# Optimization experiments

Hardware: AMD Instinct MI355X
Metric: run time of the kernel (lower is better)

Reference implementation:

```python
import jax, jax.numpy as jnp
import numpy as np

B, S, C, H = 2, 4096, 1024, 16
DH = C // H  # 64
# diffusers: attn.scale = dim_head ** -0.5; code divides scores by scale**0.5
SCALE = 1.0 / (float(DH) ** -0.25)  # == DH ** 0.25


def setup_inputs() -> dict:
    key = jax.random.key(0)
    ks = jax.random.split(key, 6)
    w = 0.02
    return {
        "hidden_states": jax.random.normal(ks[0], (B, S, C), jnp.float32),
        "Wq": jax.random.normal(ks[1], (C, C), jnp.float32) * w,
        "Wk": jax.random.normal(ks[2], (C, C), jnp.float32) * w,
        "Wv": jax.random.normal(ks[3], (C, C), jnp.float32) * w,
        "Wo": jax.random.normal(ks[4], (C, C), jnp.float32) * w,
        "bo": jnp.zeros((C,), jnp.float32),
        # token sizes >= 1 (number of patches each token represents)
        "token_sizes": jax.random.randint(ks[5], (B, S), 1, 17, jnp.int32),
    }


def _split_heads(x):
    # [B, S, C] -> [B, H, S, DH]
    return x.reshape(B, S, H, DH).transpose(0, 2, 1, 3)


def reference(hidden_states, Wq, Wk, Wv, Wo, bo, token_sizes):
    q = _split_heads(hidden_states @ Wq)  # [B,H,S,DH]
    k = _split_heads(hidden_states @ Wk)
    v = _split_heads(hidden_states @ Wv)
    # QK^T with diffusers-style scaling: scores / attn.scale**0.5 == scores * DH**0.25
    scores = jnp.einsum("bhqd,bhkd->bhqk", q, k) * SCALE  # [B,H,S,S]
    # additive log(token_size) bias over keys (self-attention path)
    log_sizes = jnp.log(token_sizes.astype(jnp.float32))  # [B,S]
    scores = scores + log_sizes[:, None, None, :]
    probs = jax.nn.softmax(scores, axis=-1)
    out = jnp.einsum("bhqk,bhkd->bhqd", probs, v)  # [B,H,S,DH]
    out = out.transpose(0, 2, 1, 3).reshape(B, S, C)  # merge heads
    return out @ Wo + bo  # to_out[0] linear; to_out[1] dropout is identity
```

## Files before the change

### kernel.cpp

```cpp
#include <hip/hip_runtime.h>


typedef unsigned short u16;
typedef unsigned int u32;
typedef _Float16 f16x8 __attribute__((ext_vector_type(8)));
typedef float f32x4 __attribute__((ext_vector_type(4)));
typedef short short4v __attribute__((ext_vector_type(4)));

constexpr int SEQ = 4096, CDIM = 1024, NH = 16, DHE = 64;
constexpr float SCALE2 = 2.8284271247461903f * 1.4426950408889634f;

template <int N> struct IC { static constexpr int v = N; };

union Frag { f16x8 v; short4v h[2]; };

__device__ __forceinline__ u16 f2h(float f) {
  union { _Float16 h; u16 u; } x;
  x.h = (_Float16)f;
  return x.u;
}

__device__ __forceinline__ u32 pkrtz(float a, float b) {
  u32 r;
  asm("v_cvt_pkrtz_f16_f32 %0, %1, %2" : "=v"(r) : "v"(a), "v"(b));
  return r;
}

__device__ __forceinline__ short4v pk4(const f32x4& v) {
  union { u32 w[2]; short4v s; } u;
  u.w[0] = pkrtz(v[0], v[1]);
  u.w[1] = pkrtz(v[2], v[3]);
  return u.s;
}

__device__ __forceinline__ float exp2fast(float x) {
  float r;
  asm("v_exp_f32 %0, %1" : "=v"(r) : "v"(x));
  return r;
}

__device__ __forceinline__ f32x4 mfma16(const Frag& a, const Frag& b, f32x4 c) {
  return __builtin_amdgcn_mfma_f32_16x16x32_f16(a.v, b.v, c, 0, 0, 0);
}

__device__ __forceinline__ void gl16(const void* g, void* l) {
  __builtin_amdgcn_global_load_lds(
      (const __attribute__((address_space(1))) u32*)g,
      (__attribute__((address_space(3))) u32*)l, 16, 0, 0);
}


__global__ void cast_x_kernel(const float* __restrict__ x, u16* __restrict__ out) {
  size_t i = ((size_t)blockIdx.x * 256 + threadIdx.x) * 8;
  float4 a = *(const float4*)(x + i);
  float4 b = *(const float4*)(x + i + 4);
  uint4 o;
  o.x = (u32)f2h(a.x) | ((u32)f2h(a.y) << 16);
  o.y = (u32)f2h(a.z) | ((u32)f2h(a.w) << 16);
  o.z = (u32)f2h(b.x) | ((u32)f2h(b.y) << 16);
  o.w = (u32)f2h(b.z) | ((u32)f2h(b.w) << 16);
  *(uint4*)(out + i) = o;
}

__global__ __launch_bounds__(256) void transpose_w4_kernel(
    const float* __restrict__ Wq, const float* __restrict__ Wk,
    const float* __restrict__ Wv, const float* __restrict__ Wo,
    u16* __restrict__ dq, u16* __restrict__ dk,
    u16* __restrict__ dv, u16* __restrict__ dow) {
  __shared__ float tile[64][65];
  const float* src;
  u16* dst;
  switch (blockIdx.z) {
    case 0: src = Wq; dst = dq; break;
    case 1: src = Wk; dst = dk; break;
    case 2: src = Wv; dst = dv; break;
    default: src = Wo; dst = dow; break;
  }
  const int r0 = blockIdx.y * 64, c0 = blockIdx.x * 64;
  const int tx = threadIdx.x & 63, ty = threadIdx.x >> 6;
#pragma unroll
  for (int i = 0; i < 16; ++i) {
    const int row = i * 4 + ty;
    tile[row][tx] = src[(size_t)(r0 + row) * 1024 + c0 + tx];
  }
  __syncthreads();
#pragma unroll
  for (int i = 0; i < 16; ++i) {
    const int row = i * 4 + ty;
    dst[(size_t)(c0 + row) * 1024 + r0 + tx] = f2h(tile[tx][row]);
  }
}

__global__ void tscast_kernel(const int* __restrict__ ts, u16* __restrict__ out) {
  int i = blockIdx.x * 256 + threadIdx.x;
  out[i] = f2h((float)ts[i]);
}


template <int EPI, int NBX>
__global__ __launch_bounds__(256) void gemm_f16(const u16* __restrict__ A,
                                                const u16* __restrict__ Bt,
                                                void* __restrict__ Out,
                                                const float* __restrict__ bias,
                                                const int* __restrict__ ts) {
  __shared__ __align__(16) short Alds[128 * 32];
  __shared__ __align__(16) short Blds[128 * 32];
  const int t = threadIdx.x;
  const int fid = blockIdx.x + NBX * blockIdx.y;
  constexpr int CPX = NBX * 64 / 8;
  const int wid = (fid & 7) * CPX + (fid >> 3);
  const int bnb = wid % NBX;
  const int bm = wid / NBX;
  const int lane = t & 63, wv = t >> 6;
  const int wm = wv >> 1, wn = wv & 1;
  const int l16 = lane & 15, lq = lane >> 4;

  f32x4 acc[4][4];
  f32x4 z = {0.f, 0.f, 0.f, 0.f};
#pragma unroll
  for (int i = 0; i < 4; ++i)
#pragma unroll
    for (int j = 0; j < 4; ++j) acc[i][j] = z;

  const int srow = t >> 2;
  const int schunk = (t & 3) ^ ((t >> 3) & 3);
  const u16* Ag = A + (size_t)(bm * 128 + srow) * 1024 + schunk * 8;
  const u16* Bg = Bt + (size_t)(bnb * 128 + srow) * 1024 + schunk * 8;
  short* Ad = Alds + (t >> 6) * 512;
  short* Bd = Blds + (t >> 6) * 512;

  const int m2 = (l16 >> 1) & 3;
  const int o0 = (((lq >> 1) ^ m2) * 8) + (lq & 1) * 4;
  const int o1 = ((((lq >> 1) | 2) ^ m2) * 8) + (lq & 1) * 4;

  for (int kb = 0; kb < 32; ++kb) {
    const int k0 = kb * 32;
    gl16(Ag + k0, Ad);
    gl16(Ag + 64 * 1024 + k0, Ad + 2048);
    gl16(Bg + k0, Bd);
    gl16(Bg + 64 * 1024 + k0, Bd + 2048);
    __syncthreads();

    Frag af[4], bf[4];
#pragma unroll
    for (int am = 0; am < 4; ++am) {
      const short* p = Alds + (wm * 64 + am * 16 + l16) * 32;
      af[am].h[0] = *(const short4v*)(p + o0);
      af[am].h[1] = *(const short4v*)(p + o1);
    }
#pragma unroll
    for (int bn = 0; bn < 4; ++bn) {
      const short* p = Blds + (wn * 64 + bn * 16 + l16) * 32;
      bf[bn].h[0] = *(const short4v*)(p + o0);
      bf[bn].h[1] = *(const short4v*)(p + o1);
    }
#pragma unroll
    for (int am = 0; am < 4; ++am)
#pragma unroll
      for (int bn = 0; bn < 4; ++bn) acc[am][bn] = mfma16(af[am], bf[bn], acc[am][bn]);
    __syncthreads();
  }

#pragma unroll
  for (int am = 0; am < 4; ++am) {
#pragma unroll
    for (int bn = 0; bn < 4; ++bn) {
#pragma unroll
      for (int r = 0; r < 4; ++r) {
        const int m = bm * 128 + wm * 64 + am * 16 + lq * 4 + r;
        const int n = bnb * 128 + wn * 64 + bn * 16 + l16;
        float vsum = acc[am][bn][r];
        if (EPI == 0) {
          const int which = n >> 10;
          const int nn = n & 1023;
          const int h = nn >> 6, d = nn & 63;
          const int b = m >> 12, s = m & 4095;
          const int bhh = b * NH + h;
          size_t addr;
          if (which == 2) {
            vsum *= (float)ts[b * SEQ + s];
            addr = (size_t)2 * 8388608 + ((size_t)bhh * DHE + d) * SEQ + s;
          } else {
            if (which == 0) vsum *= SCALE2;
            addr = (size_t)which * 8388608 + ((size_t)bhh * SEQ + s) * DHE + d;
          }
          ((u16*)Out)[addr] = f2h(vsum);
        } else {
          ((float*)Out)[(size_t)m * 1024 + n] = vsum + bias[n];
        }
      }
    }
  }
}


__global__ __launch_bounds__(256, 2) void attn_kernel(const u16* __restrict__ Q,
                                                      const u16* __restrict__ K,
                                                      const u16* __restrict__ Vt,
                                                      const u16* __restrict__ ts16,
                                                      u16* __restrict__ Out) {
  __shared__ __align__(16) short Klds[2][64][72];
  __shared__ __align__(16) short Vtlds[2][64][72];

  const int t = threadIdx.x;
  const int bid = (blockIdx.x & 7) * 64 + (blockIdx.x >> 3);
  const int bh = bid >> 4;
  const int qb = bid & 15;
  const int lane = t & 63, wv = t >> 6;
  const int l16 = lane & 15, lq = lane >> 4;
  const int b = bh >> 4, h = bh & 15;

  Frag qf[4][2];
#pragma unroll
  for (int qh = 0; qh < 4; ++qh) {
    const int qrow = qb * 256 + wv * 64 + qh * 16 + l16;
    const u16* qp = Q + ((size_t)bh * SEQ + qrow) * DHE;
#pragma unroll
    for (int f = 0; f < 2; ++f) {
      qf[qh][f].h[0] = *(const short4v*)(qp + f * 32 + lq * 4);
      qf[qh][f].h[1] = *(const short4v*)(qp + f * 32 + lq * 4 + 16);
    }
  }

  float mrow[4] = {0.f, 0.f, 0.f, 0.f};
  f32x4 lsum[4];
  f32x4 oacc[4][4];
  f32x4 z = {0.f, 0.f, 0.f, 0.f};
#pragma unroll
  for (int qh = 0; qh < 4; ++qh) {
    lsum[qh] = z;
#pragma unroll
    for (int d = 0; d < 4; ++d) oacc[qh][d] = z;
  }

  const int a7 = t & 7, sd = a7 * 8, skey = t >> 3;
  const int vd = t >> 2, voct = (t & 3) * 8;
  const int vsw = ((vd >> 3) & 7) << 3;

  const u16* Kbase = K + (size_t)bh * SEQ * DHE;
  const u16* Vtbase = Vt + ((size_t)bh * DHE + vd) * SEQ;
  const u16* tsb = ts16 + b * SEQ;

  uint4 kv0 = *(const uint4*)(Kbase + (size_t)skey * DHE + sd);
  uint4 kv1 = *(const uint4*)(Kbase + (size_t)(skey + 32) * DHE + sd);
  uint4 vv0 = *(const uint4*)(Vtbase + voct);
  uint4 vv1 = *(const uint4*)(Vtbase + voct + 32);

  Frag tsfr[2];
  Frag paf[4][2];
  f32x4 scA[4], scB[4];

  for (int kt = 0; kt < 64; ++kt) {
    short (*Kb)[72] = Klds[kt & 1];
    short (*Vb)[72] = Vtlds[kt & 1];
    *(uint4*)&Kb[skey][sd] = kv0;
    *(uint4*)&Kb[skey + 32][sd] = kv1;
    *(uint4*)&Vb[vd][voct ^ vsw] = vv0;
    *(uint4*)&Vb[vd][(voct + 32) ^ vsw] = vv1;

    if (kt < 63) {
      const u16* Kn = Kbase + (size_t)(kt + 1) * 64 * DHE + (size_t)skey * DHE + sd;
      kv0 = *(const uint4*)(Kn);
      kv1 = *(const uint4*)(Kn + 32 * DHE);
      const u16* Vn = Vtbase + (kt + 1) * 64 + voct;
      vv0 = *(const uint4*)(Vn);
      vv1 = *(const uint4*)(Vn + 32);
    }
    __syncthreads();

    {
      const u16* tst = tsb + kt * 64;
#pragma unroll
      for (int kh = 0; kh < 2; ++kh) {
        tsfr[kh].h[0] = *(const short4v*)(tst + kh * 32 + lq * 4);
        tsfr[kh].h[1] = *(const short4v*)(tst + kh * 32 + lq * 4 + 16);
      }
    }

    Frag kfr[4][2];
#pragma unroll
    for (int k2 = 0; k2 < 4; ++k2) {
#pragma unroll
      for (int f = 0; f < 2; ++f) {
        const short* p = &Kb[k2 * 16 + l16][f * 32 + lq * 4];
        kfr[k2][f].h[0] = *(const short4v*)p;
        kfr[k2][f].h[1] = *(const short4v*)(p + 16);
      }
    }

    auto qkq = [&](auto qc, f32x4 (&sc)[4]) {
      constexpr int qh = decltype(qc)::v;
      const float nm = -mrow[qh];
      f32x4 seed = {nm, nm, nm, nm};
#pragma unroll
      for (int k2 = 0; k2 < 4; ++k2) {
        f32x4 a = mfma16(kfr[k2][0], qf[qh][0], seed);
        sc[k2] = mfma16(kfr[k2][1], qf[qh][1], a);
      }
    };

    auto smq = [&](auto qc, f32x4 (&sc)[4]) {
      constexpr int qh = decltype(qc)::v;
      float hm[4];
#pragma unroll
      for (int k2 = 0; k2 < 4; ++k2) {
        const f32x4 s = sc[k2];
        hm[k2] = fmaxf(fmaxf(s[0], s[1]), fmaxf(s[2], s[3]));
      }
      float mx = fmaxf(fmaxf(hm[0], hm[1]), fmaxf(hm[2], hm[3]));
      mx = fmaxf(mx, __shfl_xor(mx, 16));
      mx = fmaxf(mx, __shfl_xor(mx, 32));
      if (__any(mx > 8.f)) {
        const float sh = fmaxf(mx, 0.f);
        const float al = exp2fast(-sh);
        mrow[qh] += sh;
        f32x4 alv;
#pragma unroll
        for (int r = 0; r < 4; ++r) alv[r] = __shfl(al, lq * 4 + r, 16);
#pragma unroll
        for (int dd = 0; dd < 4; ++dd) oacc[qh][dd] *= alv;
        lsum[qh] *= alv;
#pragma unroll
        for (int k2 = 0; k2 < 4; ++k2) sc[k2] -= sh;
      }
#pragma unroll
      for (int k2 = 0; k2 < 4; ++k2) {
        f32x4 s = sc[k2];
#pragma unroll
        for (int r = 0; r < 4; ++r) s[r] = exp2fast(s[r]);
        sc[k2] = s;
      }
      paf[qh][0].h[0] = pk4(sc[0]); paf[qh][0].h[1] = pk4(sc[1]);
      paf[qh][1].h[0] = pk4(sc[2]); paf[qh][1].h[1] = pk4(sc[3]);
      lsum[qh] = mfma16(paf[qh][0], tsfr[0], lsum[qh]);
      lsum[qh] = mfma16(paf[qh][1], tsfr[1], lsum[qh]);
    };

    qkq(IC<0>{}, scA);
    qkq(IC<1>{}, scB);
    smq(IC<0>{}, scA);
    qkq(IC<2>{}, scA);
    smq(IC<1>{}, scB);
    qkq(IC<3>{}, scB);
    smq(IC<2>{}, scA);
    smq(IC<3>{}, scB);

    __builtin_amdgcn_s_setprio(1);
#pragma unroll
    for (int dd = 0; dd < 4; ++dd) {
      const int vrow = dd * 16 + l16;
      const int e = ((vrow >> 3) & 7) << 3;
#pragma unroll
      for (int kh = 0; kh < 2; ++kh) {
        Frag vb;
        vb.h[0] = *(const short4v*)&Vb[vrow][(kh * 32 + lq * 4) ^ e];
        vb.h[1] = *(const short4v*)&Vb[vrow][(kh * 32 + 16 + lq * 4) ^ e];
#pragma unroll
        for (int qh = 0; qh < 4; ++qh)
          oacc[qh][dd] = mfma16(paf[qh][kh], vb, oacc[qh][dd]);
      }
    }
    __builtin_amdgcn_s_setprio(0);
  }

#pragma unroll
  for (int qh = 0; qh < 4; ++qh) {
    f32x4 linv;
#pragma unroll
    for (int r = 0; r < 4; ++r) linv[r] = 1.f / lsum[qh][r];
#pragma unroll
    for (int dd = 0; dd < 4; ++dd) {
#pragma unroll
      for (int r = 0; r < 4; ++r) {
        const int row = qb * 256 + wv * 64 + qh * 16 + lq * 4 + r;
        const float v = oacc[qh][dd][r] * linv[r];
        Out[((size_t)b * SEQ + row) * CDIM + h * DHE + dd * 16 + l16] = f2h(v);
      }
    }
  }
}


extern "C" void kernel_launch(void* const* d_in, const int* in_sizes, int n_in,
                              void* d_out, int out_size, void* d_ws, size_t ws_size,
                              hipStream_t stream) {
  const float* hs = (const float*)d_in[0];
  const float* Wq = (const float*)d_in[1];
  const float* Wk = (const float*)d_in[2];
  const float* Wv = (const float*)d_in[3];
  const float* Wo = (const float*)d_in[4];
  const float* bo = (const float*)d_in[5];
  const int* ts = (const int*)d_in[6];
  float* out = (float*)d_out;

  char* ws = (char*)d_ws;
  u16* xf = (u16*)(ws);
  u16* wtq = (u16*)(ws + 16777216);
  u16* wtk = (u16*)(ws + 18874368);
  u16* wtv = (u16*)(ws + 20971520);
  u16* wto = (u16*)(ws + 23068672);
  u16* qbuf = (u16*)(ws + 25165824);
  u16* kbuf = (u16*)(ws + 41943040);
  u16* vtbuf = (u16*)(ws + 58720256);
  u16* ts16 = (u16*)(ws + 75497472);

  cast_x_kernel<<<4096, 256, 0, stream>>>(hs, xf);
  transpose_w4_kernel<<<dim3(16, 16, 4), 256, 0, stream>>>(Wq, Wk, Wv, Wo,
                                                           wtq, wtk, wtv, wto);
  tscast_kernel<<<32, 256, 0, stream>>>(ts, ts16);

  gemm_f16<0, 24><<<dim3(24, 64), 256, 0, stream>>>(xf, wtq, (void*)qbuf, nullptr, ts);

  attn_kernel<<<512, 256, 0, stream>>>(qbuf, kbuf, vtbuf, ts16, xf);

  gemm_f16<1, 8><<<dim3(8, 64), 256, 0, stream>>>(xf, wto, (void*)out, bo, nullptr);

  (void)in_sizes; (void)n_in; (void)out_size; (void)ws_size;
}
```

Measured before the change: 329.4 us.

## Split attention key range across two warp groups per block with LDS merge

Doubles the attention block to 512 threads, with two 256-thread groups each processing half of the key sequence for the same query tile using separate LDS double buffers. At the end, group 1 writes its partial output, row sums and row maxima to shared memory and group 0 merges them with rescaling before normalizing and storing. This split-K style approach raises the number of waves available for latency hiding without adding blocks. In exchange it adds a reduction phase with several barriers, and launch_bounds(512,4) may squeeze registers enough to cause spills.

```diff
diff --git a/kernel.cpp b/kernel.cpp
--- a/kernel.cpp
+++ b/kernel.cpp
@@ -194,26 +194,29 @@
 }
 
 
-__global__ __launch_bounds__(256, 2) void attn_kernel(const u16* __restrict__ Q,
+__global__ __launch_bounds__(512, 4) void attn_kernel(const u16* __restrict__ Q,
                                                       const u16* __restrict__ K,
                                                       const u16* __restrict__ Vt,
                                                       const u16* __restrict__ ts16,
                                                       u16* __restrict__ Out) {
-  __shared__ __align__(16) short Klds[2][64][72];
-  __shared__ __align__(16) short Vtlds[2][64][72];
+  __shared__ __align__(16) short Klds[2][2][64][72];
+  __shared__ __align__(16) short Vtlds[2][2][64][72];
 
   const int t = threadIdx.x;
   const int bid = (blockIdx.x & 7) * 64 + (blockIdx.x >> 3);
   const int bh = bid >> 4;
   const int qb = bid & 15;
-  const int lane = t & 63, wv = t >> 6;
+  const int lane = t & 63;
+  const int grp = t >> 8;
+  const int tg = t & 255;
+  const int wvg = (t >> 6) & 3;
   const int l16 = lane & 15, lq = lane >> 4;
   const int b = bh >> 4, h = bh & 15;
 
   Frag qf[4][2];
 #pragma unroll
   for (int qh = 0; qh < 4; ++qh) {
-    const int qrow = qb * 256 + wv * 64 + qh * 16 + l16;
+    const int qrow = qb * 256 + wvg * 64 + qh * 16 + l16;
     const u16* qp = Q + ((size_t)bh * SEQ + qrow) * DHE;
 #pragma unroll
     for (int f = 0; f < 2; ++f) {
@@ -233,13 +236,14 @@
     for (int d = 0; d < 4; ++d) oacc[qh][d] = z;
   }
 
-  const int a7 = t & 7, sd = a7 * 8, skey = t >> 3;
-  const int vd = t >> 2, voct = (t & 3) * 8;
+  const int a7 = tg & 7, sd = a7 * 8, skey = tg >> 3;
+  const int vd = tg >> 2, voct = (tg & 3) * 8;
   const int vsw = ((vd >> 3) & 7) << 3;
 
-  const u16* Kbase = K + (size_t)bh * SEQ * DHE;
-  const u16* Vtbase = Vt + ((size_t)bh * DHE + vd) * SEQ;
-  const u16* tsb = ts16 + b * SEQ;
+  const int keyoff = grp * 2048;
+  const u16* Kbase = K + (size_t)bh * SEQ * DHE + (size_t)keyoff * DHE;
+  const u16* Vtbase = Vt + ((size_t)bh * DHE + vd) * SEQ + keyoff;
+  const u16* tsb = ts16 + b * SEQ + keyoff;
 
   uint4 kv0 = *(const uint4*)(Kbase + (size_t)skey * DHE + sd);
   uint4 kv1 = *(const uint4*)(Kbase + (size_t)(skey + 32) * DHE + sd);
@@ -250,15 +254,15 @@
   Frag paf[4][2];
   f32x4 scA[4], scB[4];
 
-  for (int kt = 0; kt < 64; ++kt) {
-    short (*Kb)[72] = Klds[kt & 1];
-    short (*Vb)[72] = Vtlds[kt & 1];
+  for (int kt = 0; kt < 32; ++kt) {
+    short (*Kb)[72] = Klds[grp][kt & 1];
+    short (*Vb)[72] = Vtlds[grp][kt & 1];
     *(uint4*)&Kb[skey][sd] = kv0;
     *(uint4*)&Kb[skey + 32][sd] = kv1;
     *(uint4*)&Vb[vd][voct ^ vsw] = vv0;
     *(uint4*)&Vb[vd][(voct + 32) ^ vsw] = vv1;
 
-    if (kt < 63) {
+    if (kt < 31) {
       const u16* Kn = Kbase + (size_t)(kt + 1) * 64 * DHE + (size_t)skey * DHE + sd;
       kv0 = *(const uint4*)(Kn);
       kv1 = *(const uint4*)(Kn + 32 * DHE);
@@ -363,18 +367,54 @@
     __builtin_amdgcn_s_setprio(0);
   }
 
+  float* sm = (float*)&Klds[0][0][0][0];
 #pragma unroll
   for (int qh = 0; qh < 4; ++qh) {
-    f32x4 linv;
-#pragma unroll
-    for (int r = 0; r < 4; ++r) linv[r] = 1.f / lsum[qh][r];
-#pragma unroll
-    for (int dd = 0; dd < 4; ++dd) {
+    __syncthreads();
+    if (grp == 1) {
+      float* po = sm + (wvg * 64 + lane) * 16;
+#pragma unroll
+      for (int dd = 0; dd < 4; ++dd) *(f32x4*)(po + dd * 4) = oacc[qh][dd];
+      *(f32x4*)(sm + 4096 + (wvg * 64 + lane) * 4) = lsum[qh];
+      if (lq == 0) sm[5120 + wvg * 16 + l16] = mrow[qh];
+    }
+    __syncthreads();
+    if (grp == 0) {
+      const float mB = sm[5120 + wvg * 16 + l16];
+      const float mA = mrow[qh];
+      const float mx = fmaxf(mA, mB);
+      const float aA = exp2fast(mA - mx), aB = exp2fast(mB - mx);
+      f32x4 aAr, aBr;
 #pragma unroll
       for (int r = 0; r < 4; ++r) {
-        const int row = qb * 256 + wv * 64 + qh * 16 + lq * 4 + r;
-        const float v = oacc[qh][dd][r] * linv[r];
-        Out[((size_t)b * SEQ + row) * CDIM + h * DHE + dd * 16 + l16] = f2h(v);
+        aAr[r] = __shfl(aA, lq * 4 + r, 16);
+        aBr[r] = __shfl(aB, lq * 4 + r, 16);
+      }
+      const float* po = sm + (wvg * 64 + lane) * 16;
+      f32x4 lB = *(const f32x4*)(sm + 4096 + (wvg * 64 + lane) * 4);
+      lsum[qh] = lsum[qh] * aAr + lB * aBr;
+#pragma unroll
+      for (int dd = 0; dd < 4; ++dd) {
+        f32x4 oB = *(const f32x4*)(po + dd * 4);
+        oacc[qh][dd] = oacc[qh][dd] * aAr + oB * aBr;
+      }
+    }
+  }
+
+  if (grp == 0) {
+#pragma unroll
+    for (int qh = 0; qh < 4; ++qh) {
+      f32x4 linv;
+#pragma unroll
+      for (int r = 0; r < 4; ++r) linv[r] = 1.f / lsum[qh][r];
+#pragma unroll
+      for (int dd = 0; dd < 4; ++dd) {
+#pragma unroll
+        for (int r = 0; r < 4; ++r) {
+          const int row = qb * 256 + wvg * 64 + qh * 16 + lq * 4 + r;
+          const float v = oacc[qh][dd][r] * linv[r];
+          Out[((size_t)b * SEQ + row) * CDIM + h * DHE + dd * 16 + l16] = f2h(v);
+        }
       }
     }
   }
@@ -411,7 +451,7 @@
 
   gemm_f16<0, 24><<<dim3(24, 64), 256, 0, stream>>>(xf, wtq, (void*)qbuf, nullptr, ts);
 
-  attn_kernel<<<512, 256, 0, stream>>>(qbuf, kbuf, vtbuf, ts16, xf);
+  attn_kernel<<<512, 512, 0, stream>>>(qbuf, kbuf, vtbuf, ts16, xf);
 
   gemm_f16<1, 8><<<dim3(8, 64), 256, 0, stream>>>(xf, wto, (void*)out, bo, nullptr);
 
```

Result: slower. 1.314 ms (+299.0%).
